# Kernel tuning notes

Hardware: AMD Instinct MI355X
Metric: run time of the kernel (lower is better)

The kernel has to match this reference:

```python
import jax, jax.numpy as jnp
import numpy as np

NMS_KS = 15
TOP_K = 2048
GAUSS_KS = 7
GAUSS_SIGMA = 1.0
LOSS_LAMBDA = 1.0


def setup_inputs() -> dict:
    key = jax.random.key(0)
    k1, k2, k3 = jax.random.split(key, 3)
    B, H, W = 16, 1024, 1024
    score1 = jax.random.uniform(k1, (B, 1, H, W), dtype=jnp.float32)
    w_score2 = jax.random.uniform(k2, (B, 1, H, W), dtype=jnp.float32)
    w_vis_mask2 = jax.random.randint(k3, (B, 1, H, W), 0, 2) > 0
    return {"score1": score1, "w_score2": w_score2, "w_vis_mask2": w_vis_mask2}


def _nms(score, ks):
    # keep only local maxima within a ks x ks window (stride 1, 'same' padding)
    pooled = jax.lax.reduce_window(score, -jnp.inf, jax.lax.max,
                                   (1, 1, ks, ks), (1, 1, 1, 1), 'SAME')
    return jnp.where(score == pooled, score, jnp.zeros_like(score))


def _prepare_gt_score(score, nms_ks, k, mask):
    # NMS -> mask -> per-image top-k -> binary GT keypoint map
    s = _nms(score, nms_ks) * mask.astype(score.dtype)
    b = s.shape[0]
    flat = s.reshape(b, -1)                      # B x (H*W)
    _, idx = jax.lax.top_k(flat, k)              # B x k
    gt = jnp.zeros_like(flat).at[jnp.arange(b)[:, None], idx].set(1.0)
    return gt.reshape(s.shape)


def _gaussian_filter(x, ks, sigma):
    coords = jnp.arange(ks, dtype=jnp.float32) - (ks - 1) / 2.0
    g = jnp.exp(-(coords ** 2) / (2.0 * sigma ** 2))
    g = g / g.sum()
    k2d = jnp.outer(g, g)[None, None]
    pad = ks // 2
    return jax.lax.conv_general_dilated(
        x, k2d, (1, 1), [(pad, pad), (pad, pad)],
        dimension_numbers=('NCHW', 'OIHW', 'NCHW'))


def reference(score1, w_score2, w_vis_mask2):
    b = score1.shape[0]
    gt_score1 = jax.lax.stop_gradient(
        _prepare_gt_score(w_score2, NMS_KS, TOP_K, w_vis_mask2))
    gt_score1 = _gaussian_filter(gt_score1, GAUSS_KS, GAUSS_SIGMA)
    m = w_vis_mask2.astype(jnp.float32)
    loss = ((score1 - gt_score1) ** 2) * m       # masked elementwise MSE
    loss = loss.reshape(b, -1).sum(-1) / jnp.clip(m.reshape(b, -1).sum(-1), 1e-8)
    return LOSS_LAMBDA * loss.mean()
```

## Files before the change

### kernel.cpp

```cpp
#include <hip/hip_runtime.h>
#include <math.h>

#define BATCH 16
#define H 1024
#define W 1024
#define HR 46
#define CGW 20
#define CGP 21
#define NTILES 8192
#define NBANDS (NTILES * 4)
#define CAP 4096
#define TOPK 2048
#define BCW 12

struct WS {
  float pt1[NBANDS];
  int   pmc[NBANDS];
  int   band_cnt[NBANDS];
  float corr_part[BATCH * 64];
  float band_val[NBANDS * BCW];
  int   band_idx[NBANDS * BCW];
};

__constant__ float GW[7] = {
  0.004433048175f, 0.054005582623f, 0.242036229376f, 0.399050279652f,
  0.242036229376f, 0.054005582623f, 0.004433048175f
};

__device__ __forceinline__ float4 max4(float4 a, float4 b) {
  float4 r;
  r.x = fmaxf(a.x, b.x); r.y = fmaxf(a.y, b.y);
  r.z = fmaxf(a.z, b.z); r.w = fmaxf(a.w, b.w);
  return r;
}

__global__ __launch_bounds__(256, 8) void k_nms(const float* __restrict__ score1,
                                                const float* __restrict__ score2,
                                                const int* __restrict__ mask,
                                                WS* __restrict__ ws) {
  __shared__ float4 halo[HR][CGP];
  const int tid = threadIdx.x;
  const int w = tid >> 6, l = tid & 63;

  const int t = (blockIdx.x & 7) * (NTILES / 8) + (blockIdx.x >> 3);
  const int b  = t >> 9;
  const int tt = t & 511;
  const int ty0 = (tt >> 4) << 5;
  const int tx0 = (tt & 15) << 6;
  const size_t ibase = (size_t)b * ((size_t)H * W);
  const float* s2 = score2 + ibase;

  float4 st[4]; int hr_[4], hc_[4];
  #pragma unroll
  for (int k = 0; k < 4; k++) {
    int i = tid + (k << 8);
    if (i < HR * CGW) {
      int r = i / CGW, c = i - r * CGW;
      hr_[k] = r; hc_[k] = c;
      int gy = ty0 - 7 + r, gx = tx0 - 8 + (c << 2);
      const bool ok = (gy >= 0) & (gy < H) & (gx >= 0) & (gx < W);
      int gyc = min(max(gy, 0), H - 1);
      int gxc = ok ? gx : 0;
      float4 v = *(const float4*)(s2 + (size_t)gyc * W + gxc);
      if (!ok) v = make_float4(-INFINITY, -INFINITY, -INFINITY, -INFINITY);
      st[k] = v;
    }
  }
  const int rt = (w << 3) + (l >> 3);
  const int c8 = l & 7;
  const size_t pb = ibase + (size_t)(ty0 + rt) * W + tx0 + (c8 << 3);
  const float4 s1a = *(const float4*)(score1 + pb);
  const float4 s1b = *(const float4*)(score1 + pb + 4);
  const int4  mka = *(const int4*)(mask + pb);
  const int4  mkb = *(const int4*)(mask + pb + 4);

  #pragma unroll
  for (int k = 0; k < 4; k++) {
    int i = tid + (k << 8);
    if (i < HR * CGW) halo[hr_[k]][hc_[k]] = st[k];
  }

  float t1 = 0.f; int mcnt = 0; unsigned int mbits = 0;
  {
    const float sc[8] = {s1a.x, s1a.y, s1a.z, s1a.w, s1b.x, s1b.y, s1b.z, s1b.w};
    const int   mm[8] = {mka.x, mka.y, mka.z, mka.w, mkb.x, mkb.y, mkb.z, mkb.w};
    #pragma unroll
    for (int j = 0; j < 8; j++) {
      if (mm[j]) { t1 = fmaf(sc[j], sc[j], t1); mcnt++; mbits |= (1u << j); }
    }
  }
  __syncthreads();

  float4 vr0, vr1, vr2, vr3;
  int R0 = 0, cg = 0;
  if (l < 40) {
    const int r2 = l / 20;
    cg = l - r2 * 20;
    R0 = (w << 3) + (r2 << 2);
    float4 core = halo[R0 + 3][cg];
    #pragma unroll
    for (int k = 4; k <= 14; k++) core = max4(core, halo[R0 + k][cg]);
    const float4 h0 = halo[R0][cg], h1 = halo[R0 + 1][cg], h2 = halo[R0 + 2][cg];
    const float4 h15 = halo[R0 + 15][cg], h16 = halo[R0 + 16][cg], h17 = halo[R0 + 17][cg];
    const float4 p2 = h2, p1 = max4(h1, p2), p0 = max4(h0, p1);
    const float4 sf15 = h15, sf16 = max4(sf15, h16), sf17 = max4(sf16, h17);
    vr0 = max4(core, p0);
    vr1 = max4(max4(core, p1), sf15);
    vr2 = max4(max4(core, p2), sf16);
    vr3 = max4(core, sf17);
  }
  const float4 cva = halo[rt + 7][(c8 << 1) + 2];
  const float4 cvb = halo[rt + 7][(c8 << 1) + 3];
  __syncthreads();

  if (l < 40) {
    halo[R0 + 0][cg] = vr0;
    halo[R0 + 1][cg] = vr1;
    halo[R0 + 2][cg] = vr2;
    halo[R0 + 3][cg] = vr3;
  }
  __builtin_amdgcn_wave_barrier();
  asm volatile("s_waitcnt lgkmcnt(0)" ::: "memory");
  __builtin_amdgcn_sched_barrier(0);

  float r[24];
  #pragma unroll
  for (int g = 0; g < 6; g++) {
    float4 v = halo[rt][(c8 << 1) + g];
    r[4 * g + 0] = v.x; r[4 * g + 1] = v.y; r[4 * g + 2] = v.z; r[4 * g + 3] = v.w;
  }
  float core = r[8];
  #pragma unroll
  for (int k = 9; k <= 15; k++) core = fmaxf(core, r[k]);
  const float q7 = r[7];
  const float q6 = fmaxf(r[6], q7);
  const float q5 = fmaxf(r[5], q6);
  const float q4 = fmaxf(r[4], q5);
  const float q3 = fmaxf(r[3], q4);
  const float q2 = fmaxf(r[2], q3);
  const float q1 = fmaxf(r[1], q2);
  float sa[7];
  sa[0] = r[16];
  #pragma unroll
  for (int k = 1; k < 7; k++) sa[k] = fmaxf(sa[k - 1], r[16 + k]);
  float pooled[8];
  pooled[0] = fmaxf(core, q1);
  pooled[1] = fmaxf(fmaxf(core, q2), sa[0]);
  pooled[2] = fmaxf(fmaxf(core, q3), sa[1]);
  pooled[3] = fmaxf(fmaxf(core, q4), sa[2]);
  pooled[4] = fmaxf(fmaxf(core, q5), sa[3]);
  pooled[5] = fmaxf(fmaxf(core, q6), sa[4]);
  pooled[6] = fmaxf(fmaxf(core, q7), sa[5]);
  pooled[7] = fmaxf(core, sa[6]);

  const float cc[8] = {cva.x, cva.y, cva.z, cva.w, cvb.x, cvb.y, cvb.z, cvb.w};
  int cj = -1; float cv = 0.f;
  #pragma unroll
  for (int j = 0; j < 8; j++) {
    if (((mbits >> j) & 1u) && cj < 0) {
      const float s = cc[j];
      if (s == pooled[j] && s > 0.f) { cj = j; cv = s; }
    }
  }
  const int band = (t << 2) + w;
  const unsigned long long bal = __ballot(cj >= 0);
  if (cj >= 0) {
    const int pos = (int)__popcll(bal & ((1ull << l) - 1ull));
    if (pos < BCW) {
      ws->band_val[band * BCW + pos] = cv;
      ws->band_idx[band * BCW + pos] = (ty0 + rt) * W + tx0 + (c8 << 3) + cj;
    }
  }
  #pragma unroll
  for (int off = 32; off > 0; off >>= 1) {
    t1 += __shfl_down(t1, off);
    mcnt += __shfl_down(mcnt, off);
  }
  if (l == 0) {
    int nc = (int)__popcll(bal); if (nc > BCW) nc = BCW;
    ws->band_cnt[band] = nc;
    ws->pt1[band] = t1;
    ws->pmc[band] = mcnt;
  }
}

__global__ __launch_bounds__(256, 4) void k_rankstamp(const float* __restrict__ score1,
                                                      const int* __restrict__ mask,
                                                      WS* __restrict__ ws) {
  const int blk = (blockIdx.x & 7) * 128 + (blockIdx.x >> 3);
  const int b = blk >> 6;
  const int slice = blk & 63;
  __shared__ __align__(16) float sval[CAP];
  __shared__ __align__(16) int   sidx[CAP];
  __shared__ int   wt[4];
  __shared__ int   s_tot;
  __shared__ int   s_prank[4][64];
  __shared__ int   s_keys[64];
  __shared__ int   s_nk;
  __shared__ float cred[4];
  const int tid = threadIdx.x;
  const int w = tid >> 6, l = tid & 63;

  const int base = b * 2048 + tid * 8;
  int c[8]; int csum = 0;
  #pragma unroll
  for (int u = 0; u < 8; u++) {
    int x = ws->band_cnt[base + u];
    if (x > BCW) x = BCW;
    c[u] = x; csum += x;
  }
  int v = csum;
  #pragma unroll
  for (int off = 1; off < 64; off <<= 1) {
    int u2 = __shfl_up(v, off);
    if (l >= off) v += u2;
  }
  if (l == 63) wt[w] = v;
  __syncthreads();
  int wo = 0;
  #pragma unroll
  for (int k = 0; k < 4; k++) if (k < w) wo += wt[k];
  const int excl = v - csum + wo;
  if (tid == 255) {
    int tot = excl + csum;
    if (tot > CAP) tot = CAP;
    s_tot = tot;
    #pragma unroll
    for (int u = 0; u < 3; u++)
      if (tot + u < CAP) sval[tot + u] = 0.f;
  }
  int off = excl;
  #pragma unroll
  for (int u = 0; u < 8; u++) {
    const float* sv = ws->band_val + (size_t)(base + u) * BCW;
    const int*   si = ws->band_idx + (size_t)(base + u) * BCW;
    for (int j = 0; j < c[u]; j++) {
      if (off < CAP) { sval[off] = sv[j]; sidx[off] = si[j]; }
      off++;
    }
  }
  __syncthreads();

  const int n = s_tot;
  const int i0 = slice << 6;
  if (i0 >= n) {
    if (tid == 0) ws->corr_part[b * 64 + slice] = 0.f;
    return;
  }
  const int nf4 = (n + 3) >> 2;

  const float vi = sval[i0 + l];
  const int   xi = sidx[i0 + l];
  const int q = (nf4 + 3) >> 2;
  int lo = w * q; if (lo > nf4) lo = nf4;
  int hi = lo + q; if (hi > nf4) hi = nf4;
  int rank = 0;
  int j = lo;
  for (; j + 4 <= hi; j += 4) {
    #pragma unroll
    for (int u = 0; u < 4; u++) {
      const float4 vv = ((const float4*)sval)[j + u];
      const int4  iv = ((const int4*)sidx)[j + u];
      rank += (vv.x > vi) + (vv.y > vi) + (vv.z > vi) + (vv.w > vi);
      rank += (vv.x == vi && iv.x < xi);
      rank += (vv.y == vi && iv.y < xi);
      rank += (vv.z == vi && iv.z < xi);
      rank += (vv.w == vi && iv.w < xi);
    }
  }
  for (; j < hi; j++) {
    const float4 vv = ((const float4*)sval)[j];
    const int4  iv = ((const int4*)sidx)[j];
    rank += (vv.x > vi) + (vv.y > vi) + (vv.z > vi) + (vv.w > vi);
    rank += (vv.x == vi && iv.x < xi);
    rank += (vv.y == vi && iv.y < xi);
    rank += (vv.z == vi && iv.z < xi);
    rank += (vv.w == vi && iv.w < xi);
  }
  s_prank[w][l] = rank;
  __syncthreads();

  if (tid < 64) {
    const int rtot = s_prank[0][tid] + s_prank[1][tid] + s_prank[2][tid] + s_prank[3][tid];
    const bool sel = (i0 + tid < n) && (rtot < TOPK);
    const unsigned long long bal = __ballot(sel);
    if (sel) {
      const int pos = __popcll(bal & ((1ull << tid) - 1ull));
      s_keys[pos] = sidx[i0 + tid];
    }
    if (tid == 0) s_nk = (int)__popcll(bal);
  }
  __syncthreads();
  const int nk = s_nk;

  float contrib = 0.f;
  const int sub = tid & 7;
  const size_t ib2 = (size_t)b * ((size_t)H * W);
  #pragma unroll
  for (int rnd = 0; rnd < 2; rnd++) {
    const int k = (tid >> 3) + (rnd << 5);
    if (k < nk && sub < 7) {
      const int ck = s_keys[k];
      const int cy = ck >> 10, cx = ck & 1023;
      const int py = cy + sub - 3;
      const float wy = GW[sub] * ((py >= 0 && py < H) ? 1.f : 0.f);
      const int pyc = min(max(py, 0), H - 1);
      const float* s1r = score1 + ib2 + (size_t)pyc * W;
      const int*   mr  = mask   + ib2 + (size_t)pyc * W;
      #pragma unroll
      for (int dx = -3; dx <= 3; dx++) {
        const int px = cx + dx;
        const float wv = wy * GW[dx + 3] * ((px >= 0 && px < W) ? 1.f : 0.f);
        const int pxc = min(max(px, 0), W - 1);
        const float mf = (mr[pxc] != 0) ? 1.f : 0.f;
        contrib += mf * wv * (wv - 2.f * s1r[pxc]);
      }
    }
  }
  #pragma unroll
  for (int off2 = 32; off2 > 0; off2 >>= 1) contrib += __shfl_down(contrib, off2);
  if (l == 0) cred[w] = contrib;
  __syncthreads();
  if (tid == 0)
    ws->corr_part[b * 64 + slice] = (cred[0] + cred[1]) + (cred[2] + cred[3]);
}

__global__ __launch_bounds__(1024) void k_final(WS* __restrict__ ws, float* __restrict__ out) {
  const int tid = threadIdx.x;
  const int b = tid >> 6, l = tid & 63;
  __shared__ double sD[BATCH];

  double tsum = 0.0; long long msum = 0;
  const float4* pv = (const float4*)(ws->pt1 + b * 2048);
  const int4*   pm = (const int4*)(ws->pmc + b * 2048);
  #pragma unroll
  for (int k = 0; k < 8; k++) {
    const float4 f = pv[l + (k << 6)];
    const int4   m = pm[l + (k << 6)];
    tsum += (double)f.x + (double)f.y + (double)f.z + (double)f.w;
    msum += (long long)(m.x + m.y + m.z + m.w);
  }
  double csum = (double)ws->corr_part[b * 64 + l];
  #pragma unroll
  for (int off = 32; off > 0; off >>= 1) {
    tsum += __shfl_down(tsum, off);
    msum += __shfl_down(msum, off);
    csum += __shfl_down(csum, off);
  }
  if (l == 0) {
    double denom = (double)msum;
    if (denom < 1e-8) denom = 1e-8;
    sD[b] = (tsum + csum) / denom;
  }
  __syncthreads();
  if (tid == 0) {
    double acc = 0.0;
    #pragma unroll
    for (int k = 0; k < BATCH; k++) acc += sD[k];
    out[0] = (float)(acc / BATCH);
  }
}

extern "C" void kernel_launch(void* const* d_in, const int* in_sizes, int n_in,
                              void* d_out, int out_size, void* d_ws, size_t ws_size,
                              hipStream_t stream) {
  const float* score1 = (const float*)d_in[0];
  const float* score2 = (const float*)d_in[1];
  const int*   mask   = (const int*)d_in[2];
  float* out = (float*)d_out;
  WS* ws = (WS*)d_ws;

  k_nms<<<NTILES, 256, 0, stream>>>(score1, score2, mask, ws);
  k_rankstamp<<<BATCH * 64, 256, 0, stream>>>(score1, mask, ws);
  k_final<<<1, 1024, 0, stream>>>(ws, out);
}
```

Before: 88.45 us.

## Give each wave a private NMS halo to drop block-wide barriers

Each wave now loads and owns its own 22-row halo, covering its 8 output rows plus the 7-row margins, in a per-wave shared-memory slice. The block-wide __syncthreads calls are replaced with wave-level barriers. This removes cross-wave synchronisation stalls in exchange for extra redundant halo loads, since overlapping rows are fetched by several waves. It also uses more LDS per block, so the occupancy hint drops from 8 to 5.

After: 89.76 us. Within noise of the previous version (+1.5%).

```diff
diff --git a/kernel.cpp b/kernel.cpp
--- a/kernel.cpp
+++ b/kernel.cpp
@@ -4,9 +4,6 @@
 #define BATCH 16
 #define H 1024
 #define W 1024
-#define HR 46
-#define CGW 20
-#define CGP 21
 #define NTILES 8192
 #define NBANDS (NTILES * 4)
 #define CAP 4096
@@ -34,11 +31,11 @@
   return r;
 }
 
-__global__ __launch_bounds__(256, 8) void k_nms(const float* __restrict__ score1,
+__global__ __launch_bounds__(256, 5) void k_nms(const float* __restrict__ score1,
                                                 const float* __restrict__ score2,
                                                 const int* __restrict__ mask,
                                                 WS* __restrict__ ws) {
-  __shared__ float4 halo[HR][CGP];
+  __shared__ float4 halo[4][22][21];
   const int tid = threadIdx.x;
   const int w = tid >> 6, l = tid & 63;
 
@@ -47,61 +44,65 @@
   const int tt = t & 511;
   const int ty0 = (tt >> 4) << 5;
   const int tx0 = (tt & 15) << 6;
+  const int by0 = ty0 + (w << 3);
   const size_t ibase = (size_t)b * ((size_t)H * W);
   const float* s2 = score2 + ibase;
 
-  float4 st[4]; int hr_[4], hc_[4];
-  #pragma unroll
-  for (int k = 0; k < 4; k++) {
-    int i = tid + (k << 8);
-    if (i < HR * CGW) {
-      int r = i / CGW, c = i - r * CGW;
-      hr_[k] = r; hc_[k] = c;
-      int gy = ty0 - 7 + r, gx = tx0 - 8 + (c << 2);
-      const bool ok = (gy >= 0) & (gy < H) & (gx >= 0) & (gx < W);
-      int gyc = min(max(gy, 0), H - 1);
-      int gxc = ok ? gx : 0;
-      float4 v = *(const float4*)(s2 + (size_t)gyc * W + gxc);
-      if (!ok) v = make_float4(-INFINITY, -INFINITY, -INFINITY, -INFINITY);
-      st[k] = v;
-    }
-  }
-  const int rt = (w << 3) + (l >> 3);
+  const int rl = l >> 3;
   const int c8 = l & 7;
-  const size_t pb = ibase + (size_t)(ty0 + rt) * W + tx0 + (c8 << 3);
+  const size_t pb = ibase + (size_t)(by0 + rl) * W + tx0 + (c8 << 3);
   const float4 s1a = *(const float4*)(score1 + pb);
   const float4 s1b = *(const float4*)(score1 + pb + 4);
   const int4  mka = *(const int4*)(mask + pb);
   const int4  mkb = *(const int4*)(mask + pb + 4);
 
-  #pragma unroll
-  for (int k = 0; k < 4; k++) {
-    int i = tid + (k << 8);
-    if (i < HR * CGW) halo[hr_[k]][hc_[k]] = st[k];
+  float4 st[7]; int sr[7], sc[7];
+  #pragma unroll
+  for (int k = 0; k < 7; k++) {
+    const int slot = l + (k << 6);
+    if (slot < 440) {
+      const int r = slot / 20, c = slot - r * 20;
+      sr[k] = r; sc[k] = c;
+      const int gy = by0 - 7 + r, gx = tx0 - 8 + (c << 2);
+      const bool ok = (gy >= 0) & (gy < H) & (gx >= 0) & (gx < W);
+      const int gyc = min(max(gy, 0), H - 1);
+      const int gxc = ok ? gx : 0;
+      float4 v = *(const float4*)(s2 + (size_t)gyc * W + gxc);
+      if (!ok) v = make_float4(-INFINITY, -INFINITY, -INFINITY, -INFINITY);
+      st[k] = v;
+    }
   }
 
   float t1 = 0.f; int mcnt = 0; unsigned int mbits = 0;
   {
-    const float sc[8] = {s1a.x, s1a.y, s1a.z, s1a.w, s1b.x, s1b.y, s1b.z, s1b.w};
+    const float sc_[8] = {s1a.x, s1a.y, s1a.z, s1a.w, s1b.x, s1b.y, s1b.z, s1b.w};
     const int   mm[8] = {mka.x, mka.y, mka.z, mka.w, mkb.x, mkb.y, mkb.z, mkb.w};
     #pragma unroll
     for (int j = 0; j < 8; j++) {
-      if (mm[j]) { t1 = fmaf(sc[j], sc[j], t1); mcnt++; mbits |= (1u << j); }
-    }
-  }
-  __syncthreads();
+      if (mm[j]) { t1 = fmaf(sc_[j], sc_[j], t1); mcnt++; mbits |= (1u << j); }
+    }
+  }
+
+  #pragma unroll
+  for (int k = 0; k < 7; k++) {
+    const int slot = l + (k << 6);
+    if (slot < 440) halo[w][sr[k]][sc[k]] = st[k];
+  }
+  __builtin_amdgcn_wave_barrier();
+  asm volatile("s_waitcnt lgkmcnt(0)" ::: "memory");
+  __builtin_amdgcn_sched_barrier(0);
 
   float4 vr0, vr1, vr2, vr3;
   int R0 = 0, cg = 0;
   if (l < 40) {
     const int r2 = l / 20;
     cg = l - r2 * 20;
-    R0 = (w << 3) + (r2 << 2);
-    float4 core = halo[R0 + 3][cg];
-    #pragma unroll
-    for (int k = 4; k <= 14; k++) core = max4(core, halo[R0 + k][cg]);
-    const float4 h0 = halo[R0][cg], h1 = halo[R0 + 1][cg], h2 = halo[R0 + 2][cg];
-    const float4 h15 = halo[R0 + 15][cg], h16 = halo[R0 + 16][cg], h17 = halo[R0 + 17][cg];
+    R0 = r2 << 2;
+    float4 core = halo[w][R0 + 3][cg];
+    #pragma unroll
+    for (int k = 4; k <= 14; k++) core = max4(core, halo[w][R0 + k][cg]);
+    const float4 h0 = halo[w][R0][cg], h1 = halo[w][R0 + 1][cg], h2 = halo[w][R0 + 2][cg];
+    const float4 h15 = halo[w][R0 + 15][cg], h16 = halo[w][R0 + 16][cg], h17 = halo[w][R0 + 17][cg];
     const float4 p2 = h2, p1 = max4(h1, p2), p0 = max4(h0, p1);
     const float4 sf15 = h15, sf16 = max4(sf15, h16), sf17 = max4(sf16, h17);
     vr0 = max4(core, p0);
@@ -109,24 +110,26 @@
     vr2 = max4(max4(core, p2), sf16);
     vr3 = max4(core, sf17);
   }
-  const float4 cva = halo[rt + 7][(c8 << 1) + 2];
-  const float4 cvb = halo[rt + 7][(c8 << 1) + 3];
-  __syncthreads();
-
-  if (l < 40) {
-    halo[R0 + 0][cg] = vr0;
-    halo[R0 + 1][cg] = vr1;
-    halo[R0 + 2][cg] = vr2;
-    halo[R0 + 3][cg] = vr3;
-  }
+  const float4 cva = halo[w][rl + 7][(c8 << 1) + 2];
+  const float4 cvb = halo[w][rl + 7][(c8 << 1) + 3];
   __builtin_amdgcn_wave_barrier();
   asm volatile("s_waitcnt lgkmcnt(0)" ::: "memory");
   __builtin_amdgcn_sched_barrier(0);
 
+  if (l < 40) {
+    halo[w][R0 + 0][cg] = vr0;
+    halo[w][R0 + 1][cg] = vr1;
+    halo[w][R0 + 2][cg] = vr2;
+    halo[w][R0 + 3][cg] = vr3;
+  }
+  __builtin_amdgcn_wave_barrier();
+  asm volatile("s_waitcnt lgkmcnt(0)" ::: "memory");
+  __builtin_amdgcn_sched_barrier(0);
+
   float r[24];
   #pragma unroll
   for (int g = 0; g < 6; g++) {
-    float4 v = halo[rt][(c8 << 1) + g];
+    float4 v = halo[w][rl][(c8 << 1) + g];
     r[4 * g + 0] = v.x; r[4 * g + 1] = v.y; r[4 * g + 2] = v.z; r[4 * g + 3] = v.w;
   }
   float core = r[8];
@@ -168,7 +171,7 @@
     const int pos = (int)__popcll(bal & ((1ull << l) - 1ull));
     if (pos < BCW) {
       ws->band_val[band * BCW + pos] = cv;
-      ws->band_idx[band * BCW + pos] = (ty0 + rt) * W + tx0 + (c8 << 3) + cj;
+      ws->band_idx[band * BCW + pos] = (by0 + rl) * W + tx0 + (c8 << 3) + cj;
     }
   }
   #pragma unroll
```
